# Performance work log

Measured on AMD Instinct MI355X. Metric: run time of the kernel, lower is better.

Reference implementation:

```python
import jax, jax.numpy as jnp
import numpy as np

N_NODES = 50000
N_EDGES = 800000
F_IN = 64
CHANNELS = 64
ATTN_SLOPE = 0.2   # GATConv internal LeakyReLU on attention logits
OUT_SLOPE = 0.3    # wrapper's LeakyReLU(alpha=0.3)


def setup_inputs() -> dict:
    key = jax.random.key(0)
    ks = jax.random.split(key, 7)
    x = jax.random.normal(ks[0], (N_NODES, F_IN), dtype=jnp.float32)
    edge_src = jax.random.randint(ks[1], (N_EDGES,), 0, N_NODES, dtype=jnp.int64)
    edge_dst = jax.random.randint(ks[2], (N_EDGES,), 0, N_NODES, dtype=jnp.int64)
    # Learned parameters (single attention head)
    W = jax.random.normal(ks[3], (F_IN, CHANNELS), dtype=jnp.float32) / np.sqrt(F_IN)
    a_src = jax.random.normal(ks[4], (CHANNELS,), dtype=jnp.float32) / np.sqrt(CHANNELS)
    a_dst = jax.random.normal(ks[5], (CHANNELS,), dtype=jnp.float32) / np.sqrt(CHANNELS)
    b = jnp.zeros((CHANNELS,), dtype=jnp.float32)
    return {"x": x, "W": W, "a_src": a_src, "a_dst": a_dst, "b": b,
            "edge_src": edge_src, "edge_dst": edge_dst}


def reference(x, W, a_src, a_dst, b, edge_src, edge_dst):
    N = x.shape[0]
    h = x @ W                                  # [N, C] transformed features
    s_src = h @ a_src                          # [N] per-node source score
    s_dst = h @ a_dst                          # [N] per-node dest score
    # Per-edge attention logits, LeakyReLU(0.2) as in GAT
    e = jax.nn.leaky_relu(s_src[edge_src] + s_dst[edge_dst], ATTN_SLOPE)  # [E]
    # Numerically stable softmax over each destination's neighborhood
    m = jax.ops.segment_max(e, edge_dst, num_segments=N)                  # [N]
    ex = jnp.exp(e - m[edge_dst])                                         # [E]
    denom = jax.ops.segment_sum(ex, edge_dst, num_segments=N)             # [N]
    alpha = ex / jnp.maximum(denom[edge_dst], 1e-9)                       # [E]
    # Scatter-aggregate weighted neighbor features
    out = jax.ops.segment_sum(alpha[:, None] * h[edge_src], edge_dst,
                              num_segments=N) + b                         # [N, C]
    return jax.nn.leaky_relu(out, OUT_SLOPE)
```

## Files before the change

### kernel.cpp

```cpp
#include <hip/hip_runtime.h>
#include <hip/hip_fp16.h>

#define N_NODES 50000
#define N_EDGES 800000
#define CH 64
#define FT_NODES 64
#define FT_BLKS ((N_NODES + FT_NODES - 1) / FT_NODES)
#define NB 782
#define NCHK 782
#define ECHUNK 1024
#define LCAP 2048

static constexpr size_t alignup16(size_t x) { return (x + 15) & ~(size_t)15; }
static const size_t OFF_H      = 0;
static const size_t OFF_SSRC   = alignup16(OFF_H      + (size_t)N_NODES*CH*2);
static const size_t OFF_SDST   = alignup16(OFF_SSRC   + (size_t)N_NODES*4);
static const size_t OFF_HIST   = alignup16(OFF_SDST   + (size_t)N_NODES*4);
static const size_t OFF_FLAG   = alignup16(OFF_HIST   + (size_t)NCHK*NB*4);
static const size_t OFF_CB     = alignup16(OFF_FLAG   + (size_t)NB*4);
static const size_t OFF_ROWPTR = alignup16(OFF_CB     + (size_t)(NB+1)*4);
static const size_t OFF_BUCK   = alignup16(OFF_ROWPTR + (size_t)(N_NODES+4)*4);
static const size_t OFF_SPERM  = alignup16(OFF_BUCK   + (size_t)N_EDGES*4);

__global__ __launch_bounds__(256) void k_feat(
        const float* __restrict__ x, const float* __restrict__ W,
        const float* __restrict__ a_src, const float* __restrict__ a_dst,
        const int* __restrict__ edst,
        __half* __restrict__ h, float* __restrict__ ssrc, float* __restrict__ sdst,
        unsigned int* __restrict__ hist) {
    __shared__ float Ws[64 * 64];
    __shared__ float xs[FT_NODES][68];
    __shared__ unsigned int lh[NB];
    const int tid = threadIdx.x;
    for (int j = tid; j < NB; j += 256) lh[j] = 0u;
#pragma unroll
    for (int i = 0; i < 16; ++i) Ws[tid + i * 256] = W[tid + i * 256];
    const int n0 = blockIdx.x * FT_NODES;
    const int nvalid = min(FT_NODES, N_NODES - n0);
    const float4* x4 = (const float4*)(x + (size_t)n0 * CH);
    for (int i = tid; i < nvalid * 16; i += 256) {
        const int n = i >> 4, q = i & 15;
        *(float4*)&xs[n][q * 4] = x4[i];
    }
    __syncthreads();
    {
        const int st = blockIdx.x * ECHUNK;
        const int en = min(st + ECHUNK, N_EDGES);
        const int nq = (en - st) >> 2;
        if (tid < nq) {
            const int4 d4 = *(const int4*)&edst[st + 4 * tid];
            atomicAdd(&lh[((unsigned int)d4.x) >> 6], 1u);
            atomicAdd(&lh[((unsigned int)d4.y) >> 6], 1u);
            atomicAdd(&lh[((unsigned int)d4.z) >> 6], 1u);
            atomicAdd(&lh[((unsigned int)d4.w) >> 6], 1u);
        }
    }
    const int nl = tid >> 3;
    const int g = tid & 7;
    const int c0 = g * 8;
    const int nodeA = n0 + 2 * nl;
    const bool vA = (2 * nl < nvalid);
    const bool vB = (2 * nl + 1 < nvalid);
    float accA[8] = {0,0,0,0,0,0,0,0};
    float accB[8] = {0,0,0,0,0,0,0,0};
#pragma unroll
    for (int k = 0; k < 64; ++k) {
        const float xv0 = xs[2 * nl][k];
        const float xv1 = xs[2 * nl + 1][k];
        const float4 w0 = *(const float4*)&Ws[k * 64 + c0];
        const float4 w1 = *(const float4*)&Ws[k * 64 + c0 + 4];
        accA[0] = fmaf(xv0, w0.x, accA[0]); accB[0] = fmaf(xv1, w0.x, accB[0]);
        accA[1] = fmaf(xv0, w0.y, accA[1]); accB[1] = fmaf(xv1, w0.y, accB[1]);
        accA[2] = fmaf(xv0, w0.z, accA[2]); accB[2] = fmaf(xv1, w0.z, accB[2]);
        accA[3] = fmaf(xv0, w0.w, accA[3]); accB[3] = fmaf(xv1, w0.w, accB[3]);
        accA[4] = fmaf(xv0, w1.x, accA[4]); accB[4] = fmaf(xv1, w1.x, accB[4]);
        accA[5] = fmaf(xv0, w1.y, accA[5]); accB[5] = fmaf(xv1, w1.y, accB[5]);
        accA[6] = fmaf(xv0, w1.z, accA[6]); accB[6] = fmaf(xv1, w1.z, accB[6]);
        accA[7] = fmaf(xv0, w1.w, accA[7]); accB[7] = fmaf(xv1, w1.w, accB[7]);
    }
    float psA = 0.f, pdA = 0.f, psB = 0.f, pdB = 0.f;
#pragma unroll
    for (int i = 0; i < 8; ++i) {
        const float as = a_src[c0 + i], ad = a_dst[c0 + i];
        psA = fmaf(accA[i], as, psA); pdA = fmaf(accA[i], ad, pdA);
        psB = fmaf(accB[i], as, psB); pdB = fmaf(accB[i], ad, pdB);
    }
#pragma unroll
    for (int off = 4; off; off >>= 1) {
        psA += __shfl_xor(psA, off); pdA += __shfl_xor(pdA, off);
        psB += __shfl_xor(psB, off); pdB += __shfl_xor(pdB, off);
    }
    if (vA) {
        __half2 hv[4];
#pragma unroll
        for (int i = 0; i < 4; ++i) hv[i] = __floats2half2_rn(accA[2 * i], accA[2 * i + 1]);
        *(float4*)(h + (size_t)nodeA * CH + c0) = *(float4*)hv;
        if (g == 0) { ssrc[nodeA] = psA; sdst[nodeA] = pdA; }
    }
    if (vB) {
        __half2 hv[4];
#pragma unroll
        for (int i = 0; i < 4; ++i) hv[i] = __floats2half2_rn(accB[2 * i], accB[2 * i + 1]);
        *(float4*)(h + (size_t)(nodeA + 1) * CH + c0) = *(float4*)hv;
        if (g == 0) { ssrc[nodeA + 1] = psB; sdst[nodeA + 1] = pdB; }
    }
    __syncthreads();
    for (int j = tid; j < NB; j += 256)
        hist[(size_t)blockIdx.x * NB + j] = lh[j];
}

__global__ __launch_bounds__(256) void k_scanhist(
        unsigned int* __restrict__ hist, unsigned int* __restrict__ cb,
        unsigned int* __restrict__ flags) {
    __shared__ unsigned int lcol[784];
    __shared__ unsigned int red[256];
    __shared__ unsigned int sc[256];
    const int t = threadIdx.x, b = blockIdx.x;
    for (int c = t; c < 784; c += 256)
        lcol[c] = (c < NCHK) ? hist[(size_t)c * NB + b] : 0u;
    __syncthreads();
    unsigned int v = 0u;
    for (int c = t; c < NCHK; c += 256) v += lcol[c];
    red[t] = v;
    __syncthreads();
#pragma unroll
    for (int off = 128; off; off >>= 1) {
        if (t < off) red[t] += red[t + off];
        __syncthreads();
    }
    const unsigned int total = red[0];
    if (t == 0) atomicExch(&flags[b], total | 0x40000000u);
    unsigned int pre = 0u;
    for (int j = t; j < b; j += 256) {
        unsigned int f;
        do { f = atomicAdd(&flags[j], 0u); } while ((f >> 20) != 0x400u);
        pre += f & 0xFFFFFu;
    }
    __syncthreads();
    red[t] = pre;
    __syncthreads();
#pragma unroll
    for (int off = 128; off; off >>= 1) {
        if (t < off) red[t] += red[t + off];
        __syncthreads();
    }
    const unsigned int cbb = red[0];
    if (t == 0) { cb[b] = cbb; if (b == NB - 1) cb[NB] = N_EDGES; }
    unsigned int part = 0u;
    const int c0 = 4 * t;
    if (t < 196) {
#pragma unroll
        for (int q = 0; q < 4; ++q) part += lcol[c0 + q];
    }
    sc[t] = part;
    __syncthreads();
#pragma unroll
    for (int off = 1; off < 256; off <<= 1) {
        unsigned int u = (t >= off) ? sc[t - off] : 0u;
        __syncthreads();
        sc[t] += u;
        __syncthreads();
    }
    if (t < 196) {
        unsigned int run = cbb + sc[t] - part;
#pragma unroll
        for (int q = 0; q < 4; ++q) {
            const unsigned int tmp = lcol[c0 + q];
            lcol[c0 + q] = run;
            run += tmp;
        }
    }
    __syncthreads();
    for (int c = t; c < NCHK; c += 256) hist[(size_t)c * NB + b] = lcol[c];
}

__global__ __launch_bounds__(256) void k_scatter(
        const int* __restrict__ esrc, const int* __restrict__ edst,
        const unsigned int* __restrict__ hist, unsigned int* __restrict__ buck) {
    __shared__ unsigned int wp[NB];
    const int t = threadIdx.x, blk = blockIdx.x;
    for (int j = t; j < NB; j += 256) wp[j] = hist[(size_t)blk * NB + j];
    __syncthreads();
    const int st = blk * ECHUNK;
    const int en = min(st + ECHUNK, N_EDGES);
    const int nq = (en - st) >> 2;
    if (t < nq) {
        const int4 d4 = *(const int4*)&edst[st + 4 * t];
        const int4 s4 = *(const int4*)&esrc[st + 4 * t];
        unsigned int p;
        p = atomicAdd(&wp[((unsigned int)d4.x) >> 6], 1u);
        buck[p] = (((unsigned int)d4.x) << 16) | (unsigned int)s4.x;
        p = atomicAdd(&wp[((unsigned int)d4.y) >> 6], 1u);
        buck[p] = (((unsigned int)d4.y) << 16) | (unsigned int)s4.y;
        p = atomicAdd(&wp[((unsigned int)d4.z) >> 6], 1u);
        buck[p] = (((unsigned int)d4.z) << 16) | (unsigned int)s4.z;
        p = atomicAdd(&wp[((unsigned int)d4.w) >> 6], 1u);
        buck[p] = (((unsigned int)d4.w) << 16) | (unsigned int)s4.w;
    }
}

__global__ __launch_bounds__(256) void k_csr(
        const unsigned int* __restrict__ buck, const unsigned int* __restrict__ cb,
        int* __restrict__ row_ptr, unsigned short* __restrict__ src_perm) {
    __shared__ unsigned int cnt[64];
    __shared__ unsigned int wp[64];
    __shared__ unsigned short lsrc[LCAP];
    const int t = threadIdx.x, blk = blockIdx.x;
    const int start = (int)cb[blk];
    const int end = (int)cb[blk + 1];
    const int m = end - start;
    if (t < 64) cnt[t] = 0u;
    __syncthreads();
    for (int i = start + t; i < end; i += 256)
        atomicAdd(&cnt[(buck[i] >> 16) & 63u], 1u);
    __syncthreads();
    if (t < 64) {
        const unsigned int own = cnt[t];
        unsigned int incl = own;
#pragma unroll
        for (int d = 1; d < 64; d <<= 1) {
            const unsigned int v = __shfl_up(incl, d);
            if (t >= d) incl += v;
        }
        const unsigned int excl = incl - own;
        wp[t] = excl;
        const int node = blk * 64 + t;
        if (node <= N_NODES) row_ptr[node] = start + (int)excl;
    }
    __syncthreads();
    if (m <= LCAP) {
        for (int i = start + t; i < end; i += 256) {
            const unsigned int rec = buck[i];
            const unsigned int pos = atomicAdd(&wp[(rec >> 16) & 63u], 1u);
            lsrc[pos] = (unsigned short)(rec & 0xFFFFu);
        }
        __syncthreads();
        for (int p = t; p < m; p += 256)
            src_perm[start + p] = lsrc[p];
    } else {
        for (int i = start + t; i < end; i += 256) {
            const unsigned int rec = buck[i];
            const unsigned int pos = atomicAdd(&wp[(rec >> 16) & 63u], 1u);
            src_perm[start + (int)pos] = (unsigned short)(rec & 0xFFFFu);
        }
    }
}

__global__ __launch_bounds__(256) void k_node_agg(
        const unsigned short* __restrict__ src_perm, const int* __restrict__ row_ptr,
        const float* __restrict__ ssrc, const float* __restrict__ sdst,
        const __half* __restrict__ h, const float* __restrict__ b,
        float* __restrict__ out) {
    const int tid = threadIdx.x;
    const int lane = tid & 63;
    const int wid = tid >> 6;
    const int half = lane >> 5;
    const int hl = lane & 31;
    const int slot = hl >> 4;
    const int c4 = hl & 15;
    const int node = blockIdx.x * 8 + wid * 2 + half;
    const int row = row_ptr[node];
    const int deg = row_ptr[node + 1] - row;
    const float sd = sdst[node];
    const int degmax = max(deg, __shfl_xor(deg, 32));
    float4 acc = make_float4(0.f, 0.f, 0.f, 0.f);
    float wsum = 0.f;
    for (int base = 0; base < degmax; base += 32) {
        const int j = base + hl;
        int s = 0;
        float w = 0.f;
        if (j < deg) {
            s = (int)src_perm[row + j];
            float e = ssrc[s] + sd;
            e = (e > 0.f) ? e : 0.2f * e;
            w = __expf(e);
        }
        wsum += w;
        const int cnt_t = min(32, degmax - base);
        for (int j2 = 0; j2 < cnt_t; j2 += 16) {
            float a[8]; int si[8]; float2 raw[8];
#pragma unroll
            for (int q = 0; q < 8; ++q) {
                const int srcl = half * 32 + j2 + 2 * q + slot;
                a[q] = __shfl(w, srcl);
                si[q] = __shfl(s, srcl);
            }
#pragma unroll
            for (int q = 0; q < 8; ++q)
                raw[q] = *(const float2*)&h[(size_t)si[q] * CH + 4 * c4];
#pragma unroll
            for (int q = 0; q < 8; ++q) {
                union { float2 f2; __half2 h2[2]; } u;
                u.f2 = raw[q];
                const float2 lo = __half22float2(u.h2[0]);
                const float2 hi = __half22float2(u.h2[1]);
                acc.x = fmaf(a[q], lo.x, acc.x);
                acc.y = fmaf(a[q], lo.y, acc.y);
                acc.z = fmaf(a[q], hi.x, acc.z);
                acc.w = fmaf(a[q], hi.y, acc.w);
            }
        }
    }
    acc.x += __shfl_xor(acc.x, 16);
    acc.y += __shfl_xor(acc.y, 16);
    acc.z += __shfl_xor(acc.z, 16);
    acc.w += __shfl_xor(acc.w, 16);
#pragma unroll
    for (int off = 16; off; off >>= 1) wsum += __shfl_xor(wsum, off);
    if (hl < 16) {
        const float inv = 1.f / fmaxf(wsum, 1e-9f);
        const float4 bb = *(const float4*)&b[4 * c4];
        float vx = acc.x * inv + bb.x;
        float vy = acc.y * inv + bb.y;
        float vz = acc.z * inv + bb.z;
        float vw = acc.w * inv + bb.w;
        vx = (vx > 0.f) ? vx : 0.3f * vx;
        vy = (vy > 0.f) ? vy : 0.3f * vy;
        vz = (vz > 0.f) ? vz : 0.3f * vz;
        vw = (vw > 0.f) ? vw : 0.3f * vw;
        *(float4*)&out[(size_t)node * CH + 4 * c4] = make_float4(vx, vy, vz, vw);
    }
}

extern "C" void kernel_launch(void* const* d_in, const int* in_sizes, int n_in,
                              void* d_out, int out_size, void* d_ws, size_t ws_size,
                              hipStream_t stream) {
    const float* x     = (const float*)d_in[0];
    const float* W     = (const float*)d_in[1];
    const float* a_src = (const float*)d_in[2];
    const float* a_dst = (const float*)d_in[3];
    const float* b     = (const float*)d_in[4];
    const int* esrc    = (const int*)d_in[5];
    const int* edst    = (const int*)d_in[6];
    float* out = (float*)d_out;

    char* ws = (char*)d_ws;
    __half* h                = (__half*)(ws + OFF_H);
    float* ssrc              = (float*)(ws + OFF_SSRC);
    float* sdst              = (float*)(ws + OFF_SDST);
    unsigned int* hist       = (unsigned int*)(ws + OFF_HIST);
    unsigned int* flags      = (unsigned int*)(ws + OFF_FLAG);
    unsigned int* cb         = (unsigned int*)(ws + OFF_CB);
    int* row_ptr             = (int*)(ws + OFF_ROWPTR);
    unsigned int* buck       = (unsigned int*)(ws + OFF_BUCK);
    unsigned short* src_perm = (unsigned short*)(ws + OFF_SPERM);

    k_feat<<<FT_BLKS, 256, 0, stream>>>(x, W, a_src, a_dst, edst, h, ssrc, sdst, hist);
    k_scanhist<<<NB, 256, 0, stream>>>(hist, cb, flags);
    k_scatter<<<NCHK, 256, 0, stream>>>(esrc, edst, hist, buck);
    k_csr<<<NB, 256, 0, stream>>>(buck, cb, row_ptr, src_perm);
    k_node_agg<<<N_NODES / 8, 256, 0, stream>>>(src_perm, row_ptr, ssrc, sdst, h, b, out);
}
```

Baseline: 69.85 us.

## Fuse scatter and CSR kernels using per-bucket completion counters

Merges the bucket scatter and per-bucket CSR build into one kernel. Each block publishes how many edges it wrote into each bucket via atomic counters, then spins until its own bucket is complete before building the CSR segment. This removes one kernel launch and the grid-wide boundary between the two phases. It relies on all 782 blocks being co-resident, since otherwise the spin-wait could deadlock. The final src_perm store is also widened to 32-bit writes.

Result: slower. 246.6 us (+253.0%).

```diff
diff --git a/kernel.cpp b/kernel.cpp
--- a/kernel.cpp
+++ b/kernel.cpp
@@ -17,7 +17,8 @@
 static const size_t OFF_SDST   = alignup16(OFF_SSRC   + (size_t)N_NODES*4);
 static const size_t OFF_HIST   = alignup16(OFF_SDST   + (size_t)N_NODES*4);
 static const size_t OFF_FLAG   = alignup16(OFF_HIST   + (size_t)NCHK*NB*4);
-static const size_t OFF_CB     = alignup16(OFF_FLAG   + (size_t)NB*4);
+static const size_t OFF_DONE   = alignup16(OFF_FLAG   + (size_t)NB*4);
+static const size_t OFF_CB     = alignup16(OFF_DONE   + (size_t)NB*4);
 static const size_t OFF_ROWPTR = alignup16(OFF_CB     + (size_t)(NB+1)*4);
 static const size_t OFF_BUCK   = alignup16(OFF_ROWPTR + (size_t)(N_NODES+4)*4);
 static const size_t OFF_SPERM  = alignup16(OFF_BUCK   + (size_t)N_EDGES*4);
@@ -111,11 +112,12 @@
 
 __global__ __launch_bounds__(256) void k_scanhist(
         unsigned int* __restrict__ hist, unsigned int* __restrict__ cb,
-        unsigned int* __restrict__ flags) {
+        unsigned int* __restrict__ flags, unsigned int* __restrict__ done) {
     __shared__ unsigned int lcol[784];
     __shared__ unsigned int red[256];
     __shared__ unsigned int sc[256];
     const int t = threadIdx.x, b = blockIdx.x;
+    if (t == 0) atomicExch(&done[b], 0u);
     for (int c = t; c < 784; c += 256)
         lcol[c] = (c < NCHK) ? hist[(size_t)c * NB + b] : 0u;
     __syncthreads();
@@ -174,12 +176,23 @@
     for (int c = t; c < NCHK; c += 256) hist[(size_t)c * NB + b] = lcol[c];
 }
 
-__global__ __launch_bounds__(256) void k_scatter(
+__global__ __launch_bounds__(256) void k_scatcsr(
         const int* __restrict__ esrc, const int* __restrict__ edst,
-        const unsigned int* __restrict__ hist, unsigned int* __restrict__ buck) {
+        const unsigned int* __restrict__ hist, const unsigned int* __restrict__ cb,
+        unsigned int* __restrict__ done, unsigned int* __restrict__ buck,
+        int* __restrict__ row_ptr, unsigned short* __restrict__ src_perm) {
+    __shared__ unsigned int wbase[NB];
     __shared__ unsigned int wp[NB];
+    __shared__ unsigned int cnt[64];
+    __shared__ unsigned int wpn[64];
+    __shared__ unsigned short lsrc[LCAP];
     const int t = threadIdx.x, blk = blockIdx.x;
-    for (int j = t; j < NB; j += 256) wp[j] = hist[(size_t)blk * NB + j];
+
+    for (int j = t; j < NB; j += 256) {
+        const unsigned int base = hist[(size_t)blk * NB + j];
+        wbase[j] = base;
+        wp[j] = base;
+    }
     __syncthreads();
     const int st = blk * ECHUNK;
     const int en = min(st + ECHUNK, N_EDGES);
@@ -197,18 +210,21 @@
         p = atomicAdd(&wp[((unsigned int)d4.w) >> 6], 1u);
         buck[p] = (((unsigned int)d4.w) << 16) | (unsigned int)s4.w;
     }
-}
-
-__global__ __launch_bounds__(256) void k_csr(
-        const unsigned int* __restrict__ buck, const unsigned int* __restrict__ cb,
-        int* __restrict__ row_ptr, unsigned short* __restrict__ src_perm) {
-    __shared__ unsigned int cnt[64];
-    __shared__ unsigned int wp[64];
-    __shared__ unsigned short lsrc[LCAP];
-    const int t = threadIdx.x, blk = blockIdx.x;
+    __threadfence();
+    __syncthreads();
+    for (int j = t; j < NB; j += 256) {
+        const unsigned int d = wp[j] - wbase[j];
+        if (d) atomicAdd(&done[j], d);
+    }
+
     const int start = (int)cb[blk];
     const int end = (int)cb[blk + 1];
     const int m = end - start;
+    if (t == 0) {
+        while (atomicAdd(&done[blk], 0u) < (unsigned int)m) { }
+    }
+    __syncthreads();
+    __threadfence();
     if (t < 64) cnt[t] = 0u;
     __syncthreads();
     for (int i = start + t; i < end; i += 256)
@@ -223,7 +239,7 @@
             if (t >= d) incl += v;
         }
         const unsigned int excl = incl - own;
-        wp[t] = excl;
+        wpn[t] = excl;
         const int node = blk * 64 + t;
         if (node <= N_NODES) row_ptr[node] = start + (int)excl;
     }
@@ -231,16 +247,22 @@
     if (m <= LCAP) {
         for (int i = start + t; i < end; i += 256) {
             const unsigned int rec = buck[i];
-            const unsigned int pos = atomicAdd(&wp[(rec >> 16) & 63u], 1u);
+            const unsigned int pos = atomicAdd(&wpn[(rec >> 16) & 63u], 1u);
             lsrc[pos] = (unsigned short)(rec & 0xFFFFu);
         }
         __syncthreads();
-        for (int p = t; p < m; p += 256)
-            src_perm[start + p] = lsrc[p];
+        int p0 = 0;
+        if (start & 1) { if (t == 0 && m > 0) src_perm[start] = lsrc[0]; p0 = 1; }
+        const int pairs = (m - p0) >> 1;
+        unsigned int* dst32 = (unsigned int*)(src_perm + start + p0);
+        for (int p = t; p < pairs; p += 256)
+            dst32[p] = (unsigned int)lsrc[p0 + 2 * p] |
+                       ((unsigned int)lsrc[p0 + 2 * p + 1] << 16);
+        if (((m - p0) & 1) && t == 0) src_perm[start + m - 1] = lsrc[m - 1];
     } else {
         for (int i = start + t; i < end; i += 256) {
             const unsigned int rec = buck[i];
-            const unsigned int pos = atomicAdd(&wp[(rec >> 16) & 63u], 1u);
+            const unsigned int pos = atomicAdd(&wpn[(rec >> 16) & 63u], 1u);
             src_perm[start + (int)pos] = (unsigned short)(rec & 0xFFFFu);
         }
     }
@@ -340,14 +362,14 @@
     float* sdst              = (float*)(ws + OFF_SDST);
     unsigned int* hist       = (unsigned int*)(ws + OFF_HIST);
     unsigned int* flags      = (unsigned int*)(ws + OFF_FLAG);
+    unsigned int* done       = (unsigned int*)(ws + OFF_DONE);
     unsigned int* cb         = (unsigned int*)(ws + OFF_CB);
     int* row_ptr             = (int*)(ws + OFF_ROWPTR);
     unsigned int* buck       = (unsigned int*)(ws + OFF_BUCK);
     unsigned short* src_perm = (unsigned short*)(ws + OFF_SPERM);
 
     k_feat<<<FT_BLKS, 256, 0, stream>>>(x, W, a_src, a_dst, edst, h, ssrc, sdst, hist);
-    k_scanhist<<<NB, 256, 0, stream>>>(hist, cb, flags);
-    k_scatter<<<NCHK, 256, 0, stream>>>(esrc, edst, hist, buck);
-    k_csr<<<NB, 256, 0, stream>>>(buck, cb, row_ptr, src_perm);
+    k_scanhist<<<NB, 256, 0, stream>>>(hist, cb, flags, done);
+    k_scatcsr<<<NB, 256, 0, stream>>>(esrc, edst, hist, cb, done, buck, row_ptr, src_perm);
     k_node_agg<<<N_NODES / 8, 256, 0, stream>>>(src_perm, row_ptr, ssrc, sdst, h, b, out);
 }
```
